# Performance work log

Measured on AMD Instinct MI355X. Metric: run time of the kernel, lower is better.

Reference implementation:

```python
import jax, jax.numpy as jnp
import numpy as np

EPS = 1e-12  # torch F.normalize eps

def setup_inputs() -> dict:
    key = jax.random.key(0)
    k1, k2, k3, k4 = jax.random.split(key, 4)
    bs, n_tok, in_dim = 64, 2048, 1024   # in_dim = 2*time_dim
    expert_dim, n_experts = 256, 512     # n_experts == 'channels' in the torch code
    x = jax.random.normal(k1, (bs, n_tok, in_dim), dtype=jnp.float32)
    W = jax.random.normal(k2, (expert_dim, in_dim), dtype=jnp.float32) * (1.0 / np.sqrt(in_dim))
    b = jax.random.normal(k3, (expert_dim,), dtype=jnp.float32) * 0.01
    centers = jax.random.normal(k4, (n_experts, expert_dim), dtype=jnp.float32)
    return {"x": x, "W": W, "b": b, "centers": centers, "top_k": 2}

def _l2norm(v):
    return v / jnp.maximum(jnp.linalg.norm(v, axis=-1, keepdims=True), EPS)

def reference(x, W, b, centers, top_k):
    # projection: (bs, n, in_dim) @ (in_dim, expert_dim)
    x_proj = jnp.einsum('bni,ei->bne', x, W) + b
    x_proj = _l2norm(x_proj)
    c = _l2norm(centers)                       # (n_experts, expert_dim)
    cosine_sim = jnp.einsum('bnd,ed->bne', x_proj, c)  # (bs, n, n_experts)
    topk_vals, topk_idx = jax.lax.top_k(cosine_sim, top_k)
    topk_probs = jax.nn.softmax(topk_vals, axis=-1)
    return topk_probs, topk_idx
```

## Files before the change

kernel.cpp:

```cpp
#include <hip/hip_runtime.h>
#include <math.h>

#define IN_DIM 1024
#define E_DIM  256
#define N_EXP  512
#define N_TOK  131072
#define TM     32
#define BK     16
#define NT     64
#define BUF_BYTES 18432

typedef double d4 __attribute__((ext_vector_type(4)));

__device__ __forceinline__ void ins2(double v, int c,
                                     double& v1, int& i1, double& v2, int& i2)
{
    if (v > v1 || (v == v1 && c < i1)) { v2 = v1; i2 = i1; v1 = v; i1 = c; }
    else if (v > v2 || (v == v2 && c < i2)) { v2 = v; i2 = c; }
}

__device__ __forceinline__ void gload_lds16(const float* g, float* l)
{
    __builtin_amdgcn_global_load_lds(
        (const __attribute__((address_space(1))) unsigned int*)(g),
        (__attribute__((address_space(3))) unsigned int*)(l),
        16, 0, 0);
}

__global__ __launch_bounds__(64) void center_norm_kernel(
    const float* __restrict__ centers, double* __restrict__ cTd)
{
    const int ctr  = blockIdx.x;
    const int lane = threadIdx.x;
    const float* row = centers + (size_t)ctr * E_DIM;
    double v[4];
    double s = 0.0;
#pragma unroll
    for (int i = 0; i < 4; ++i) { v[i] = (double)row[lane + 64 * i]; s = fma(v[i], v[i], s); }
#pragma unroll
    for (int off = 32; off >= 1; off >>= 1) s += __shfl_xor(s, off, 64);
    const double inv = 1.0 / fmax(sqrt(s), 1e-12);
#pragma unroll
    for (int i = 0; i < 4; ++i)
        cTd[(size_t)(lane + 64 * i) * N_EXP + ctr] = v[i] * inv;
}

__global__ __launch_bounds__(256, 2) void router_kernel(
    const float* __restrict__ x, const float* __restrict__ W,
    const float* __restrict__ bias, const double* __restrict__ cTd,
    float* __restrict__ out)
{
    __shared__ __align__(16) char smem_raw[65536];
    const int tid  = threadIdx.x;
    const int lane = tid & 63;
    const int wv   = tid >> 6;
    const int r    = lane & 15;
    const int q    = lane >> 4;
    const int tokBase = blockIdx.x * TM;

    const int srow = lane >> 2;
    const int scol = (lane & 3) ^ ((lane >> 3) & 3);
    const float* xg = x + (size_t)(tokBase + (wv & 1) * 16 + srow) * IN_DIM + scol * 4;
    const float* wg = W + (size_t)(wv * 16 + srow) * IN_DIM + scol * 4;

    d4 acc[2][4];
#pragma unroll
    for (int m = 0; m < 2; ++m)
#pragma unroll
        for (int n = 0; n < 4; ++n) acc[m][n] = (d4){0.0, 0.0, 0.0, 0.0};

    const int swz   = (r >> 1) & 3;
    const int abase = r * 16 + q;
    const int bbase = (wv * 64 + r) * 16 + q;

    {
        float* b = (float*)smem_raw;
        if (wv < 2) gload_lds16(xg, b + wv * 256);
#pragma unroll
        for (int p = 0; p < 4; ++p)
            gload_lds16(wg + (size_t)p * 64 * IN_DIM, b + 512 + p * 1024 + wv * 256);
    }
    __syncthreads();

    int cur = 0;
    for (int t = 0; t < NT; ++t) {
        if (t + 1 < NT) {
            float* b = (float*)(smem_raw + (cur ^ 1) * BUF_BYTES);
            const int k0 = (t + 1) * BK;
            if (wv < 2) gload_lds16(xg + k0, b + wv * 256);
#pragma unroll
            for (int p = 0; p < 4; ++p)
                gload_lds16(wg + (size_t)p * 64 * IN_DIM + k0, b + 512 + p * 1024 + wv * 256);
        }
        const float* xb = (const float*)(smem_raw + cur * BUF_BYTES);
        const float* wb = xb + 512;
#pragma unroll
        for (int kk = 0; kk < 4; ++kk) {
            const int so = 4 * (kk ^ swz);
            const double a0 = (double)xb[abase + so];
            const double a1 = (double)xb[abase + 256 + so];
#pragma unroll
            for (int n = 0; n < 4; ++n) {
                const double b = (double)wb[bbase + n * 256 + so];
                acc[0][n] = __builtin_amdgcn_mfma_f64_16x16x4f64(a0, b, acc[0][n], 0, 0, 0);
                acc[1][n] = __builtin_amdgcn_mfma_f64_16x16x4f64(a1, b, acc[1][n], 0, 0, 0);
            }
        }
        __syncthreads();
        cur ^= 1;
    }

#pragma unroll
    for (int n = 0; n < 4; ++n) {
        const double bb = (double)bias[wv * 64 + n * 16 + r];
#pragma unroll
        for (int m = 0; m < 2; ++m)
#pragma unroll
            for (int i = 0; i < 4; ++i) acc[m][n][i] += bb;
    }

    double* partials = (double*)smem_raw;
    double ss[2][4];
#pragma unroll
    for (int m = 0; m < 2; ++m)
#pragma unroll
        for (int i = 0; i < 4; ++i) {
            double s = 0.0;
#pragma unroll
            for (int n = 0; n < 4; ++n) s = fma(acc[m][n][i], acc[m][n][i], s);
#pragma unroll
            for (int off = 8; off >= 1; off >>= 1) s += __shfl_xor(s, off, 64);
            ss[m][i] = s;
        }
    if (r == 0) {
#pragma unroll
        for (int m = 0; m < 2; ++m)
#pragma unroll
            for (int i = 0; i < 4; ++i)
                partials[wv * 32 + m * 16 + q * 4 + i] = ss[m][i];
    }
    __syncthreads();

    double inv[2][4];
#pragma unroll
    for (int m = 0; m < 2; ++m)
#pragma unroll
        for (int i = 0; i < 4; ++i) {
            const int t = m * 16 + q * 4 + i;
            const double s = partials[t] + partials[32 + t] + partials[64 + t] + partials[96 + t];
            inv[m][i] = 1.0 / fmax(sqrt(s), 1e-12);
        }
    __syncthreads();

    double* projn = (double*)smem_raw;
#pragma unroll
    for (int m = 0; m < 2; ++m)
#pragma unroll
        for (int n = 0; n < 4; ++n)
#pragma unroll
            for (int i = 0; i < 4; ++i)
                projn[(wv * 64 + n * 16 + r) * 32 + m * 16 + q * 4 + i] = acc[m][n][i] * inv[m][i];
    __syncthreads();

    double tv1[2][4], tv2[2][4];
    int    ti1[2][4], ti2[2][4];
#pragma unroll
    for (int m = 0; m < 2; ++m)
#pragma unroll
        for (int i = 0; i < 4; ++i) {
            tv1[m][i] = -1e300; tv2[m][i] = -1e300; ti1[m][i] = 0; ti2[m][i] = 0;
        }

    for (int pass = 0; pass < 2; ++pass) {
        const int colbase = wv * 128 + pass * 64;
        d4 acc2[2][4];
#pragma unroll
        for (int m = 0; m < 2; ++m)
#pragma unroll
            for (int n = 0; n < 4; ++n) acc2[m][n] = (d4){0.0, 0.0, 0.0, 0.0};

        const double* cb = cTd + colbase + r;
#pragma unroll 4
        for (int kk = 0; kk < 64; ++kk) {
            const int k = kk * 4 + q;
            const double a0 = projn[k * 32 + r];
            const double a1 = projn[k * 32 + 16 + r];
#pragma unroll
            for (int n = 0; n < 4; ++n) {
                const double b = cb[(size_t)k * N_EXP + n * 16];
                acc2[0][n] = __builtin_amdgcn_mfma_f64_16x16x4f64(a0, b, acc2[0][n], 0, 0, 0);
                acc2[1][n] = __builtin_amdgcn_mfma_f64_16x16x4f64(a1, b, acc2[1][n], 0, 0, 0);
            }
        }
#pragma unroll
        for (int m = 0; m < 2; ++m)
#pragma unroll
            for (int i = 0; i < 4; ++i)
#pragma unroll
                for (int n = 0; n < 4; ++n)
                    ins2(acc2[m][n][i], colbase + n * 16 + r,
                         tv1[m][i], ti1[m][i], tv2[m][i], ti2[m][i]);
    }

#pragma unroll
    for (int m = 0; m < 2; ++m)
#pragma unroll
        for (int i = 0; i < 4; ++i) {
#pragma unroll
            for (int off = 8; off >= 1; off >>= 1) {
                const double ov1 = __shfl_xor(tv1[m][i], off, 64);
                const int    oi1 = __shfl_xor(ti1[m][i], off, 64);
                const double ov2 = __shfl_xor(tv2[m][i], off, 64);
                const int    oi2 = __shfl_xor(ti2[m][i], off, 64);
                ins2(ov1, oi1, tv1[m][i], ti1[m][i], tv2[m][i], ti2[m][i]);
                ins2(ov2, oi2, tv1[m][i], ti1[m][i], tv2[m][i], ti2[m][i]);
            }
        }

    __syncthreads();
    double* cand = (double*)smem_raw;
    if (r == 0) {
#pragma unroll
        for (int m = 0; m < 2; ++m)
#pragma unroll
            for (int i = 0; i < 4; ++i) {
                const int t = m * 16 + q * 4 + i;
                double* cd = cand + ((wv * 32 + t) << 2);
                cd[0] = tv1[m][i]; cd[1] = (double)ti1[m][i];
                cd[2] = tv2[m][i]; cd[3] = (double)ti2[m][i];
            }
    }
    __syncthreads();

    if (tid < 32) {
        double v1 = -1e300, v2 = -1e300;
        int    i1 = 0, i2 = 0;
        for (int s = 0; s < 4; ++s) {
            const double* cd = cand + ((s * 32 + tid) << 2);
            ins2(cd[0], (int)cd[1], v1, i1, v2, i2);
            ins2(cd[2], (int)cd[3], v1, i1, v2, i2);
        }
        const double e  = exp(v2 - v1);
        const double dn = 1.0 + e;
        const size_t g  = (size_t)tokBase + tid;
        out[g * 2 + 0] = (float)(1.0 / dn);
        out[g * 2 + 1] = (float)(e / dn);
        out[(size_t)2 * N_TOK + g * 2 + 0] = (float)i1;
        out[(size_t)2 * N_TOK + g * 2 + 1] = (float)i2;
    }
}

extern "C" void kernel_launch(void* const* d_in, const int* in_sizes, int n_in,
                              void* d_out, int out_size, void* d_ws, size_t ws_size,
                              hipStream_t stream)
{
    const float* x       = (const float*)d_in[0];
    const float* W       = (const float*)d_in[1];
    const float* bias    = (const float*)d_in[2];
    const float* centers = (const float*)d_in[3];
    double* cTd = (double*)d_ws;
    float*  out = (float*)d_out;

    center_norm_kernel<<<N_EXP, 64, 0, stream>>>(centers, cTd);
    router_kernel<<<N_TOK / TM, 256, 0, stream>>>(x, W, bias, cTd, out);
}
```

Before: 2.718 ms.

## Split cosine-sim stage into two 16-token halves to shrink LDS footprint

The second GEMM and top-k stage now handles the 32-token tile as two 16-token halves, staging only 16 normalized projections at a time in a padded LDS buffer (stride 17 to avoid bank conflicts). The shared allocation drops from 64KB to 36KB and the per-half accumulators and top-k state halve, cutting register and LDS pressure so more blocks can be resident. The cost is that the centers matrix is streamed from global/L2 twice per block, with extra barriers per half.

```diff
diff --git a/kernel.cpp b/kernel.cpp
--- a/kernel.cpp
+++ b/kernel.cpp
@@ -9,6 +9,9 @@
 #define BK     16
 #define NT     64
 #define BUF_BYTES 18432
+#define PJ_STR 17
+#define PJ_BYTES (E_DIM * PJ_STR * 8)
+#define SMEM_BYTES 36864
 
 typedef double d4 __attribute__((ext_vector_type(4)));
 
@@ -50,7 +53,7 @@
     const float* __restrict__ bias, const double* __restrict__ cTd,
     float* __restrict__ out)
 {
-    __shared__ __align__(16) char smem_raw[65536];
+    __shared__ __align__(16) char smem_raw[SMEM_BYTES];
     const int tid  = threadIdx.x;
     const int lane = tid & 63;
     const int wv   = tid >> 6;
@@ -119,7 +122,7 @@
             for (int i = 0; i < 4; ++i) acc[m][n][i] += bb;
     }
 
-    double* partials = (double*)smem_raw;
+    double* partials = (double*)(smem_raw + PJ_BYTES);
     double ss[2][4];
 #pragma unroll
     for (int m = 0; m < 2; ++m)
@@ -150,103 +153,92 @@
             const double s = partials[t] + partials[32 + t] + partials[64 + t] + partials[96 + t];
             inv[m][i] = 1.0 / fmax(sqrt(s), 1e-12);
         }
-    __syncthreads();
 
     double* projn = (double*)smem_raw;
-#pragma unroll
-    for (int m = 0; m < 2; ++m)
+    double* cand  = (double*)(smem_raw + PJ_BYTES);
+
+    for (int h = 0; h < 2; ++h) {
+        __syncthreads();
+
 #pragma unroll
         for (int n = 0; n < 4; ++n)
 #pragma unroll
             for (int i = 0; i < 4; ++i)
-                projn[(wv * 64 + n * 16 + r) * 32 + m * 16 + q * 4 + i] = acc[m][n][i] * inv[m][i];
-    __syncthreads();
-
-    double tv1[2][4], tv2[2][4];
-    int    ti1[2][4], ti2[2][4];
-#pragma unroll
-    for (int m = 0; m < 2; ++m)
+                projn[(wv * 64 + n * 16 + r) * PJ_STR + q * 4 + i] = acc[h][n][i] * inv[h][i];
+        __syncthreads();
+
+        double tv1[4], tv2[4];
+        int    ti1[4], ti2[4];
+#pragma unroll
+        for (int i = 0; i < 4; ++i) { tv1[i] = -1e300; tv2[i] = -1e300; ti1[i] = 0; ti2[i] = 0; }
+
+        for (int pass = 0; pass < 2; ++pass) {
+            const int colbase = wv * 128 + pass * 64;
+            d4 acc2[4];
+#pragma unroll
+            for (int n = 0; n < 4; ++n) acc2[n] = (d4){0.0, 0.0, 0.0, 0.0};
+
+            const double* pa = projn + q * PJ_STR + r;
+            const double* cb = cTd + (size_t)q * N_EXP + colbase + r;
+#pragma unroll 4
+            for (int kk = 0; kk < 64; ++kk) {
+                const double a = pa[0];
+#pragma unroll
+                for (int n = 0; n < 4; ++n) {
+                    const double b = cb[n * 16];
+                    acc2[n] = __builtin_amdgcn_mfma_f64_16x16x4f64(a, b, acc2[n], 0, 0, 0);
+                }
+                pa += 4 * PJ_STR;
+                cb += (size_t)4 * N_EXP;
+            }
+#pragma unroll
+            for (int i = 0; i < 4; ++i)
+#pragma unroll
+                for (int n = 0; n < 4; ++n)
+                    ins2(acc2[n][i], colbase + n * 16 + r,
+                         tv1[i], ti1[i], tv2[i], ti2[i]);
+        }
+
 #pragma unroll
         for (int i = 0; i < 4; ++i) {
-            tv1[m][i] = -1e300; tv2[m][i] = -1e300; ti1[m][i] = 0; ti2[m][i] = 0;
-        }
-
-    for (int pass = 0; pass < 2; ++pass) {
-        const int colbase = wv * 128 + pass * 64;
-        d4 acc2[2][4];
-#pragma unroll
-        for (int m = 0; m < 2; ++m)
-#pragma unroll
-            for (int n = 0; n < 4; ++n) acc2[m][n] = (d4){0.0, 0.0, 0.0, 0.0};
-
-        const double* cb = cTd + colbase + r;
-#pragma unroll 4
-        for (int kk = 0; kk < 64; ++kk) {
-            const int k = kk * 4 + q;
-            const double a0 = projn[k * 32 + r];
-            const double a1 = projn[k * 32 + 16 + r];
-#pragma unroll
-            for (int n = 0; n < 4; ++n) {
-                const double b = cb[(size_t)k * N_EXP + n * 16];
-                acc2[0][n] = __builtin_amdgcn_mfma_f64_16x16x4f64(a0, b, acc2[0][n], 0, 0, 0);
-                acc2[1][n] = __builtin_amdgcn_mfma_f64_16x16x4f64(a1, b, acc2[1][n], 0, 0, 0);
-            }
-        }
-#pragma unroll
-        for (int m = 0; m < 2; ++m)
-#pragma unroll
-            for (int i = 0; i < 4; ++i)
-#pragma unroll
-                for (int n = 0; n < 4; ++n)
-                    ins2(acc2[m][n][i], colbase + n * 16 + r,
-                         tv1[m][i], ti1[m][i], tv2[m][i], ti2[m][i]);
-    }
-
-#pragma unroll
-    for (int m = 0; m < 2; ++m)
-#pragma unroll
-        for (int i = 0; i < 4; ++i) {
 #pragma unroll
             for (int off = 8; off >= 1; off >>= 1) {
-                const double ov1 = __shfl_xor(tv1[m][i], off, 64);
-                const int    oi1 = __shfl_xor(ti1[m][i], off, 64);
-                const double ov2 = __shfl_xor(tv2[m][i], off, 64);
-                const int    oi2 = __shfl_xor(ti2[m][i], off, 64);
-                ins2(ov1, oi1, tv1[m][i], ti1[m][i], tv2[m][i], ti2[m][i]);
-                ins2(ov2, oi2, tv1[m][i], ti1[m][i], tv2[m][i], ti2[m][i]);
-            }
-        }
-
-    __syncthreads();
-    double* cand = (double*)smem_raw;
-    if (r == 0) {
-#pragma unroll
-        for (int m = 0; m < 2; ++m)
+                const double ov1 = __shfl_xor(tv1[i], off, 64);
+                const int    oi1 = __shfl_xor(ti1[i], off, 64);
+                const double ov2 = __shfl_xor(tv2[i], off, 64);
+                const int    oi2 = __shfl_xor(ti2[i], off, 64);
+                ins2(ov1, oi1, tv1[i], ti1[i], tv2[i], ti2[i]);
+                ins2(ov2, oi2, tv1[i], ti1[i], tv2[i], ti2[i]);
+            }
+        }
+
+        __syncthreads();
+        if (r == 0) {
 #pragma unroll
             for (int i = 0; i < 4; ++i) {
-                const int t = m * 16 + q * 4 + i;
-                double* cd = cand + ((wv * 32 + t) << 2);
-                cd[0] = tv1[m][i]; cd[1] = (double)ti1[m][i];
-                cd[2] = tv2[m][i]; cd[3] = (double)ti2[m][i];
-            }
-    }
-    __syncthreads();
-
-    if (tid < 32) {
-        double v1 = -1e300, v2 = -1e300;
-        int    i1 = 0, i2 = 0;
-        for (int s = 0; s < 4; ++s) {
-            const double* cd = cand + ((s * 32 + tid) << 2);
-            ins2(cd[0], (int)cd[1], v1, i1, v2, i2);
-            ins2(cd[2], (int)cd[3], v1, i1, v2, i2);
-        }
-        const double e  = exp(v2 - v1);
-        const double dn = 1.0 + e;
-        const size_t g  = (size_t)tokBase + tid;
-        out[g * 2 + 0] = (float)(1.0 / dn);
-        out[g * 2 + 1] = (float)(e / dn);
-        out[(size_t)2 * N_TOK + g * 2 + 0] = (float)i1;
-        out[(size_t)2 * N_TOK + g * 2 + 1] = (float)i2;
+                double* cd = cand + ((wv * 16 + q * 4 + i) << 2);
+                cd[0] = tv1[i]; cd[1] = (double)ti1[i];
+                cd[2] = tv2[i]; cd[3] = (double)ti2[i];
+            }
+        }
+        __syncthreads();
+
+        if (tid < 16) {
+            double v1 = -1e300, v2 = -1e300;
+            int    i1 = 0, i2 = 0;
+            for (int s = 0; s < 4; ++s) {
+                const double* cd = cand + ((s * 16 + tid) << 2);
+                ins2(cd[0], (int)cd[1], v1, i1, v2, i2);
+                ins2(cd[2], (int)cd[3], v1, i1, v2, i2);
+            }
+            const double e  = exp(v2 - v1);
+            const double dn = 1.0 + e;
+            const size_t g  = (size_t)tokBase + h * 16 + tid;
+            out[g * 2 + 0] = (float)(1.0 / dn);
+            out[g * 2 + 1] = (float)(e / dn);
+            out[(size_t)2 * N_TOK + g * 2 + 0] = (float)i1;
+            out[(size_t)2 * N_TOK + g * 2 + 1] = (float)i2;
+        }
     }
 }
 
```

Measured after the change: 5.158 ms. 1.9x slower.
